# Kernel optimization log

Measured on AMD Instinct MI355X. Metric: run time of the kernel, lower is better.

## Reference

```python
import jax, jax.numpy as jnp
import numpy as np

ROWS, COLS = 10, 4
B, N = 65536, 16


def setup_inputs() -> dict:
    key = jax.random.key(0)
    kx, kc = jax.random.split(key)
    # 0.5 scale keeps trace(x^(rows+1))^cols finite in float32 (spectral radius ~2)
    x = jax.random.normal(kx, (B, N, N), dtype=jnp.float32) * 0.5
    # kaiming_normal_ on a 2D (rows, cols) tensor: std = sqrt(2 / fan_in), fan_in = cols
    coef = jax.random.normal(kc, (ROWS, COLS), dtype=jnp.float32) * np.float32(np.sqrt(2.0 / COLS))
    return {"x": x, "coef": coef}


def reference(x, coef):
    # x: [B, N, N]; coef: [rows, cols]
    rows, cols = coef.shape
    n = x.shape[-1] * x.shape[-2]  # numel per sample

    A0 = jnp.matmul(x, x)  # x^2, the first a_series entry

    def step(A, _):
        # original records trace(a_series[i]) = trace(x^(i+2)), then advances the power
        tr = jnp.trace(A, axis1=-2, axis2=-1)  # [B]
        return jnp.matmul(x, A), tr

    _, traces = jax.lax.scan(step, A0, None, length=rows)  # traces: [rows, B]
    t = traces.T  # [B, rows]

    jexp = jnp.arange(1, cols + 1, dtype=jnp.float32)  # j+1 exponents
    iexp = jnp.arange(rows, dtype=jnp.float32)
    # feature[b, i, j] = trace(x^(i+2))^(j+1) / n^(i+j+1)
    denom = jnp.float32(n) ** (iexp[:, None] + jexp[None, :])  # [rows, cols]
    feats = (t[:, :, None] ** jexp[None, None, :]) / denom  # [B, rows, cols]

    # terms = coef * feats, summed over (rows, cols) per sample -> [B]
    return jnp.einsum('rc,brc->b', coef, feats)
```

## Files before the change

### kernel.cpp

```cpp
#include <hip/hip_runtime.h>

typedef __fp16 f16x4 __attribute__((ext_vector_type(4)));
typedef __fp16 f16x2 __attribute__((ext_vector_type(2)));
typedef float f32x4 __attribute__((ext_vector_type(4)));

__device__ __forceinline__ f16x4 cat(f16x2 lo, f16x2 hi) {
    return __builtin_shufflevector(lo, hi, 0, 1, 2, 3);
}
__device__ __forceinline__ f16x2 u2h(unsigned v) {
    union { unsigned u; f16x2 h; } x; x.u = v; return x.h;
}
template <int CTRL>
__device__ __forceinline__ float dpp_add(float v) {
    int s = __builtin_amdgcn_update_dpp(0, __float_as_int(v), CTRL, 0xf, 0xf, true);
    return v + __int_as_float(s);
}

__global__ __launch_bounds__(256, 8) void acoef_kernel(
    const float* __restrict__ x,
    const float* __restrict__ coef,
    float* __restrict__ out,
    int B)
{
    const int lane = threadIdx.x & 63;
    const int wid  = (blockIdx.x * 256 + threadIdx.x) >> 6;
    const int stride = gridDim.x * 4;

    const int n = lane & 15;
    const int q = lane >> 4;
    const bool diagsel = ((n >> 2) == q);

    unsigned slo = (n == 0 ? 0x3C00u : 0u) | (n == 1 ? 0x3C000000u : 0u);
    unsigned shi = (n == 2 ? 0x3C00u : 0u) | (n == 3 ? 0x3C000000u : 0u);
    const f16x4 selB  = cat(u2h(slo), u2h(shi));
    const f16x4 onesA = cat(u2h(0x3C003C00u), u2h(0x3C003C00u));
    const f32x4 zero  = {0.f, 0.f, 0.f, 0.f};
    float4 cf[3]; float scl[3];
    #pragma unroll
    for (int p = 0; p < 3; ++p) {
        int s = 4 * p + n;
        int idx = s > 9 ? 9 : s;
        cf[p]  = *(const float4*)(coef + 4 * idx);
        scl[p] = __int_as_float((127 - 8 * s) << 23);
    }

    const int aoff = n * 16 + 4 * q;
    const int boff = 4 * q * 16 + n;

    int s = wid;
    const float* xb = x + (size_t)s * 256;
    float4 a = *(const float4*)(xb + aoff);
    float b0 = xb[boff], b1 = xb[boff + 16], b2 = xb[boff + 32], b3 = xb[boff + 48];

    while (true) {
        const int s2 = s + stride;
        const bool more = (s2 < B);
        const float* xn = x + (size_t)(more ? s2 : s) * 256;
        float4 an = *(const float4*)(xn + aoff);
        float bn0 = xn[boff], bn1 = xn[boff + 16], bn2 = xn[boff + 32], bn3 = xn[boff + 48];

        f16x4 xA = cat(__builtin_amdgcn_cvt_pkrtz(a.x, a.y),
                       __builtin_amdgcn_cvt_pkrtz(a.z, a.w));
        f16x4 xB = cat(__builtin_amdgcn_cvt_pkrtz(b0, b1),
                       __builtin_amdgcn_cvt_pkrtz(b2, b3));

        f32x4 acc = __builtin_amdgcn_mfma_f32_16x16x16f16(xA, xB, zero, 0, 0, 0);

        f16x2 prpk[6];
        float trf = 0.0f;
        #pragma unroll
        for (int st = 0; st < 10; ++st) {
            float selA = (n & 1) ? acc[1] : acc[0];
            float selBv = (n & 1) ? acc[3] : acc[2];
            float dv = (n & 2) ? selBv : selA;
            float tr = diagsel ? dv : 0.0f;
            if (st & 1) prpk[st >> 1] = __builtin_amdgcn_cvt_pkrtz(trf, tr);
            else        trf = tr;

            if (st < 9) {
                f16x4 bf = cat(__builtin_amdgcn_cvt_pkrtz(acc[0], acc[1]),
                               __builtin_amdgcn_cvt_pkrtz(acc[2], acc[3]));
                acc = __builtin_amdgcn_mfma_f32_16x16x16f16(xA, bf, zero, 0, 0, 0);
            }
        }
        prpk[5] = u2h(0u);

        float result = 0.0f;
        #pragma unroll
        for (int p = 0; p < 3; ++p) {
            f16x4 Ap = cat(prpk[2 * p], prpk[2 * p + 1]);
            f32x4 c1 = __builtin_amdgcn_mfma_f32_16x16x16f16(Ap, selB, zero, 0, 0, 0);
            f16x4 Bp = cat(__builtin_amdgcn_cvt_pkrtz(c1[0], c1[1]),
                           __builtin_amdgcn_cvt_pkrtz(c1[2], c1[3]));
            f32x4 c2 = __builtin_amdgcn_mfma_f32_16x16x16f16(onesA, Bp, zero, 0, 0, 0);
            float t = c2[0];
            float sv = t * 0x1p-8f;
            float h = fmaf(sv, cf[p].w, cf[p].z);
            h = fmaf(sv, h, cf[p].y);
            h = fmaf(sv, h, cf[p].x);
            result = fmaf(sv * h, scl[p], result);
        }
        result = dpp_add<0xB1>(result);
        result = dpp_add<0x4E>(result);
        if (lane == 0) out[s] = result;

        if (!more) break;
        s = s2; a = an; b0 = bn0; b1 = bn1; b2 = bn2; b3 = bn3;
    }
}

extern "C" void kernel_launch(void* const* d_in, const int* in_sizes, int n_in,
                              void* d_out, int out_size, void* d_ws, size_t ws_size,
                              hipStream_t stream) {
    const float* x    = (const float*)d_in[0];
    const float* coef = (const float*)d_in[1];
    float* out        = (float*)d_out;
    const int B = in_sizes[0] / 256;
    acoef_kernel<<<dim3(2048), dim3(256), 0, stream>>>(x, coef, out, B);
}
```

Baseline: 96.12 us.

## Process two samples per wave to interleave independent MFMA chains

```diff
diff --git a/kernel.cpp b/kernel.cpp
--- a/kernel.cpp
+++ b/kernel.cpp
@@ -16,7 +16,7 @@
     return v + __int_as_float(s);
 }
 
-__global__ __launch_bounds__(256, 8) void acoef_kernel(
+__global__ __launch_bounds__(256, 4) void acoef_kernel(
     const float* __restrict__ x,
     const float* __restrict__ coef,
     float* __restrict__ out,
@@ -24,7 +24,7 @@
 {
     const int lane = threadIdx.x & 63;
     const int wid  = (blockIdx.x * 256 + threadIdx.x) >> 6;
-    const int stride = gridDim.x * 4;
+    const int nw   = gridDim.x * 4;
 
     const int n = lane & 15;
     const int q = lane >> 4;
@@ -45,67 +45,95 @@
     }
 
     const int aoff = n * 16 + 4 * q;
-    const int boff = 4 * q * 16 + n;
+    const int boff = 64 * q + n;
 
-    int s = wid;
-    const float* xb = x + (size_t)s * 256;
-    float4 a = *(const float4*)(xb + aoff);
-    float b0 = xb[boff], b1 = xb[boff + 16], b2 = xb[boff + 32], b3 = xb[boff + 48];
+    const int npair = B >> 1;
+    int pp = wid;
+
+    float4 a[2], bv[2];
+    {
+        const float* x0 = x + (size_t)(2 * pp) * 256;
+        const float* x1 = x0 + 256;
+        a[0]  = *(const float4*)(x0 + aoff);
+        a[1]  = *(const float4*)(x1 + aoff);
+        bv[0] = make_float4(x0[boff], x0[boff + 16], x0[boff + 32], x0[boff + 48]);
+        bv[1] = make_float4(x1[boff], x1[boff + 16], x1[boff + 32], x1[boff + 48]);
+    }
 
     while (true) {
-        const int s2 = s + stride;
-        const bool more = (s2 < B);
-        const float* xn = x + (size_t)(more ? s2 : s) * 256;
-        float4 an = *(const float4*)(xn + aoff);
-        float bn0 = xn[boff], bn1 = xn[boff + 16], bn2 = xn[boff + 32], bn3 = xn[boff + 48];
+        const int pn = pp + nw;
+        const bool more = (pn < npair);
+        const float* y0 = x + (size_t)(2 * (more ? pn : pp)) * 256;
+        const float* y1 = y0 + 256;
+        float4 na0 = *(const float4*)(y0 + aoff);
+        float4 na1 = *(const float4*)(y1 + aoff);
+        float4 nb0 = make_float4(y0[boff], y0[boff + 16], y0[boff + 32], y0[boff + 48]);
+        float4 nb1 = make_float4(y1[boff], y1[boff + 16], y1[boff + 32], y1[boff + 48]);
 
-        f16x4 xA = cat(__builtin_amdgcn_cvt_pkrtz(a.x, a.y),
-                       __builtin_amdgcn_cvt_pkrtz(a.z, a.w));
-        f16x4 xB = cat(__builtin_amdgcn_cvt_pkrtz(b0, b1),
-                       __builtin_amdgcn_cvt_pkrtz(b2, b3));
+        f16x4 xA[2], xB[2];
+        f32x4 acc[2];
+        #pragma unroll
+        for (int c = 0; c < 2; ++c) {
+            xA[c] = cat(__builtin_amdgcn_cvt_pkrtz(a[c].x, a[c].y),
+                        __builtin_amdgcn_cvt_pkrtz(a[c].z, a[c].w));
+            xB[c] = cat(__builtin_amdgcn_cvt_pkrtz(bv[c].x, bv[c].y),
+                        __builtin_amdgcn_cvt_pkrtz(bv[c].z, bv[c].w));
+            acc[c] = __builtin_amdgcn_mfma_f32_16x16x16f16(xA[c], xB[c], zero, 0, 0, 0);
+        }
 
-        f32x4 acc = __builtin_amdgcn_mfma_f32_16x16x16f16(xA, xB, zero, 0, 0, 0);
-
-        f16x2 prpk[6];
-        float trf = 0.0f;
+        f16x2 prpk[2][6];
+        float trf[2];
         #pragma unroll
         for (int st = 0; st < 10; ++st) {
-            float selA = (n & 1) ? acc[1] : acc[0];
-            float selBv = (n & 1) ? acc[3] : acc[2];
-            float dv = (n & 2) ? selBv : selA;
-            float tr = diagsel ? dv : 0.0f;
-            if (st & 1) prpk[st >> 1] = __builtin_amdgcn_cvt_pkrtz(trf, tr);
-            else        trf = tr;
-
+            #pragma unroll
+            for (int c = 0; c < 2; ++c) {
+                float sA = (n & 1) ? acc[c][1] : acc[c][0];
+                float sB = (n & 1) ? acc[c][3] : acc[c][2];
+                float dv = (n & 2) ? sB : sA;
+                float tr = diagsel ? dv : 0.0f;
+                if (st & 1) prpk[c][st >> 1] = __builtin_amdgcn_cvt_pkrtz(trf[c], tr);
+                else        trf[c] = tr;
+            }
             if (st < 9) {
-                f16x4 bf = cat(__builtin_amdgcn_cvt_pkrtz(acc[0], acc[1]),
-                               __builtin_amdgcn_cvt_pkrtz(acc[2], acc[3]));
-                acc = __builtin_amdgcn_mfma_f32_16x16x16f16(xA, bf, zero, 0, 0, 0);
+                #pragma unroll
+                for (int c = 0; c < 2; ++c) {
+                    f16x4 bf = cat(__builtin_amdgcn_cvt_pkrtz(acc[c][0], acc[c][1]),
+                                   __builtin_amdgcn_cvt_pkrtz(acc[c][2], acc[c][3]));
+                    acc[c] = __builtin_amdgcn_mfma_f32_16x16x16f16(xA[c], bf, zero, 0, 0, 0);
+                }
             }
         }
-        prpk[5] = u2h(0u);
+        prpk[0][5] = u2h(0u);
+        prpk[1][5] = u2h(0u);
 
-        float result = 0.0f;
+        float res[2] = {0.0f, 0.0f};
         #pragma unroll
         for (int p = 0; p < 3; ++p) {
-            f16x4 Ap = cat(prpk[2 * p], prpk[2 * p + 1]);
-            f32x4 c1 = __builtin_amdgcn_mfma_f32_16x16x16f16(Ap, selB, zero, 0, 0, 0);
-            f16x4 Bp = cat(__builtin_amdgcn_cvt_pkrtz(c1[0], c1[1]),
-                           __builtin_amdgcn_cvt_pkrtz(c1[2], c1[3]));
-            f32x4 c2 = __builtin_amdgcn_mfma_f32_16x16x16f16(onesA, Bp, zero, 0, 0, 0);
-            float t = c2[0];
-            float sv = t * 0x1p-8f;
-            float h = fmaf(sv, cf[p].w, cf[p].z);
-            h = fmaf(sv, h, cf[p].y);
-            h = fmaf(sv, h, cf[p].x);
-            result = fmaf(sv * h, scl[p], result);
+            #pragma unroll
+            for (int c = 0; c < 2; ++c) {
+                f16x4 Ap = cat(prpk[c][2 * p], prpk[c][2 * p + 1]);
+                f32x4 c1 = __builtin_amdgcn_mfma_f32_16x16x16f16(Ap, selB, zero, 0, 0, 0);
+                f16x4 Bp = cat(__builtin_amdgcn_cvt_pkrtz(c1[0], c1[1]),
+                               __builtin_amdgcn_cvt_pkrtz(c1[2], c1[3]));
+                f32x4 c2 = __builtin_amdgcn_mfma_f32_16x16x16f16(onesA, Bp, zero, 0, 0, 0);
+                float t = c2[0];
+                float sv = t * 0x1p-8f;
+                float h = fmaf(sv, cf[p].w, cf[p].z);
+                h = fmaf(sv, h, cf[p].y);
+                h = fmaf(sv, h, cf[p].x);
+                res[c] = fmaf(sv * h, scl[p], res[c]);
+            }
         }
-        result = dpp_add<0xB1>(result);
-        result = dpp_add<0x4E>(result);
-        if (lane == 0) out[s] = result;
+        #pragma unroll
+        for (int c = 0; c < 2; ++c) {
+            res[c] = dpp_add<0xB1>(res[c]);
+            res[c] = dpp_add<0x4E>(res[c]);
+        }
+        if (lane == 0) *(float2*)(out + 2 * pp) = make_float2(res[0], res[1]);
 
         if (!more) break;
-        s = s2; a = an; b0 = bn0; b1 = bn1; b2 = bn2; b3 = bn3;
+        pp = pn;
+        a[0] = na0; a[1] = na1; bv[0] = nb0; bv[1] = nb1;
     }
 }
 
@@ -116,5 +144,5 @@
     const float* coef = (const float*)d_in[1];
     float* out        = (float*)d_out;
     const int B = in_sizes[0] / 256;
-    acoef_kernel<<<dim3(2048), dim3(256), 0, stream>>>(x, coef, out, B);
+    acoef_kernel<<<dim3(1024), dim3(256), 0, stream>>>(x, coef, out, B);
 }
```

Measured after the change: 100.2 us. +4.2%, slower.

## Launch one wave per sample and transpose x via identity MFMA

Applied to the files above, without the earlier changes.

```diff
diff --git a/kernel.cpp b/kernel.cpp
--- a/kernel.cpp
+++ b/kernel.cpp
@@ -16,25 +16,32 @@
     return v + __int_as_float(s);
 }
 
-__global__ __launch_bounds__(256, 8) void acoef_kernel(
+__global__ __launch_bounds__(256, 6) void acoef_kernel(
     const float* __restrict__ x,
     const float* __restrict__ coef,
-    float* __restrict__ out,
-    int B)
+    float* __restrict__ out)
 {
     const int lane = threadIdx.x & 63;
-    const int wid  = (blockIdx.x * 256 + threadIdx.x) >> 6;
-    const int stride = gridDim.x * 4;
+    const int b = (blockIdx.x * 256 + (int)threadIdx.x) >> 6;
 
     const int n = lane & 15;
     const int q = lane >> 4;
     const bool diagsel = ((n >> 2) == q);
 
+    const float4 a = *(const float4*)(x + (size_t)b * 256 + n * 16 + 4 * q);
+
+    unsigned ilo = 0, ihi = 0;
+    if (diagsel) {
+        ilo = ((n & 3) == 0 ? 0x3C00u : 0u) | ((n & 3) == 1 ? 0x3C000000u : 0u);
+        ihi = ((n & 3) == 2 ? 0x3C00u : 0u) | ((n & 3) == 3 ? 0x3C000000u : 0u);
+    }
+    const f16x4 idB = cat(u2h(ilo), u2h(ihi));
     unsigned slo = (n == 0 ? 0x3C00u : 0u) | (n == 1 ? 0x3C000000u : 0u);
     unsigned shi = (n == 2 ? 0x3C00u : 0u) | (n == 3 ? 0x3C000000u : 0u);
     const f16x4 selB  = cat(u2h(slo), u2h(shi));
     const f16x4 onesA = cat(u2h(0x3C003C00u), u2h(0x3C003C00u));
     const f32x4 zero  = {0.f, 0.f, 0.f, 0.f};
+
     float4 cf[3]; float scl[3];
     #pragma unroll
     for (int p = 0; p < 3; ++p) {
@@ -44,69 +51,51 @@
         scl[p] = __int_as_float((127 - 8 * s) << 23);
     }
 
-    const int aoff = n * 16 + 4 * q;
-    const int boff = 4 * q * 16 + n;
+    f16x4 xA = cat(__builtin_amdgcn_cvt_pkrtz(a.x, a.y),
+                   __builtin_amdgcn_cvt_pkrtz(a.z, a.w));
+    f32x4 d = __builtin_amdgcn_mfma_f32_16x16x16f16(xA, idB, zero, 0, 0, 0);
+    f16x4 xB = cat(__builtin_amdgcn_cvt_pkrtz(d[0], d[1]),
+                   __builtin_amdgcn_cvt_pkrtz(d[2], d[3]));
 
-    int s = wid;
-    const float* xb = x + (size_t)s * 256;
-    float4 a = *(const float4*)(xb + aoff);
-    float b0 = xb[boff], b1 = xb[boff + 16], b2 = xb[boff + 32], b3 = xb[boff + 48];
+    f32x4 acc = __builtin_amdgcn_mfma_f32_16x16x16f16(xA, xB, zero, 0, 0, 0);
 
-    while (true) {
-        const int s2 = s + stride;
-        const bool more = (s2 < B);
-        const float* xn = x + (size_t)(more ? s2 : s) * 256;
-        float4 an = *(const float4*)(xn + aoff);
-        float bn0 = xn[boff], bn1 = xn[boff + 16], bn2 = xn[boff + 32], bn3 = xn[boff + 48];
+    f16x2 prpk[6];
+    float trf = 0.0f;
+    #pragma unroll
+    for (int st = 0; st < 10; ++st) {
+        float sA = (n & 1) ? acc[1] : acc[0];
+        float sB = (n & 1) ? acc[3] : acc[2];
+        float dv = (n & 2) ? sB : sA;
+        float tr = diagsel ? dv : 0.0f;
+        if (st & 1) prpk[st >> 1] = __builtin_amdgcn_cvt_pkrtz(trf, tr);
+        else        trf = tr;
 
-        f16x4 xA = cat(__builtin_amdgcn_cvt_pkrtz(a.x, a.y),
-                       __builtin_amdgcn_cvt_pkrtz(a.z, a.w));
-        f16x4 xB = cat(__builtin_amdgcn_cvt_pkrtz(b0, b1),
-                       __builtin_amdgcn_cvt_pkrtz(b2, b3));
+        if (st < 9) {
+            f16x4 bf = cat(__builtin_amdgcn_cvt_pkrtz(acc[0], acc[1]),
+                           __builtin_amdgcn_cvt_pkrtz(acc[2], acc[3]));
+            acc = __builtin_amdgcn_mfma_f32_16x16x16f16(xA, bf, zero, 0, 0, 0);
+        }
+    }
+    prpk[5] = u2h(0u);
 
-        f32x4 acc = __builtin_amdgcn_mfma_f32_16x16x16f16(xA, xB, zero, 0, 0, 0);
-
-        f16x2 prpk[6];
-        float trf = 0.0f;
-        #pragma unroll
-        for (int st = 0; st < 10; ++st) {
-            float selA = (n & 1) ? acc[1] : acc[0];
-            float selBv = (n & 1) ? acc[3] : acc[2];
-            float dv = (n & 2) ? selBv : selA;
-            float tr = diagsel ? dv : 0.0f;
-            if (st & 1) prpk[st >> 1] = __builtin_amdgcn_cvt_pkrtz(trf, tr);
-            else        trf = tr;
-
-            if (st < 9) {
-                f16x4 bf = cat(__builtin_amdgcn_cvt_pkrtz(acc[0], acc[1]),
-                               __builtin_amdgcn_cvt_pkrtz(acc[2], acc[3]));
-                acc = __builtin_amdgcn_mfma_f32_16x16x16f16(xA, bf, zero, 0, 0, 0);
-            }
-        }
-        prpk[5] = u2h(0u);
-
-        float result = 0.0f;
-        #pragma unroll
-        for (int p = 0; p < 3; ++p) {
-            f16x4 Ap = cat(prpk[2 * p], prpk[2 * p + 1]);
-            f32x4 c1 = __builtin_amdgcn_mfma_f32_16x16x16f16(Ap, selB, zero, 0, 0, 0);
-            f16x4 Bp = cat(__builtin_amdgcn_cvt_pkrtz(c1[0], c1[1]),
-                           __builtin_amdgcn_cvt_pkrtz(c1[2], c1[3]));
-            f32x4 c2 = __builtin_amdgcn_mfma_f32_16x16x16f16(onesA, Bp, zero, 0, 0, 0);
-            float t = c2[0];
-            float sv = t * 0x1p-8f;
-            float h = fmaf(sv, cf[p].w, cf[p].z);
-            h = fmaf(sv, h, cf[p].y);
-            h = fmaf(sv, h, cf[p].x);
-            result = fmaf(sv * h, scl[p], result);
-        }
-        result = dpp_add<0xB1>(result);
-        result = dpp_add<0x4E>(result);
-        if (lane == 0) out[s] = result;
-
-        if (!more) break;
-        s = s2; a = an; b0 = bn0; b1 = bn1; b2 = bn2; b3 = bn3;
+    float result = 0.0f;
+    #pragma unroll
+    for (int p = 0; p < 3; ++p) {
+        f16x4 Ap = cat(prpk[2 * p], prpk[2 * p + 1]);
+        f32x4 c1 = __builtin_amdgcn_mfma_f32_16x16x16f16(Ap, selB, zero, 0, 0, 0);
+        f16x4 Bp = cat(__builtin_amdgcn_cvt_pkrtz(c1[0], c1[1]),
+                       __builtin_amdgcn_cvt_pkrtz(c1[2], c1[3]));
+        f32x4 c2 = __builtin_amdgcn_mfma_f32_16x16x16f16(onesA, Bp, zero, 0, 0, 0);
+        float t = c2[0];
+        float sv = t * 0x1p-8f;
+        float h = fmaf(sv, cf[p].w, cf[p].z);
+        h = fmaf(sv, h, cf[p].y);
+        h = fmaf(sv, h, cf[p].x);
+        result = fmaf(sv * h, scl[p], result);
     }
+    result = dpp_add<0xB1>(result);
+    result = dpp_add<0x4E>(result);
+    if (lane == 0) out[b] = result;
 }
 
 extern "C" void kernel_launch(void* const* d_in, const int* in_sizes, int n_in,
@@ -116,5 +105,5 @@
     const float* coef = (const float*)d_in[1];
     float* out        = (float*)d_out;
     const int B = in_sizes[0] / 256;
-    acoef_kernel<<<dim3(2048), dim3(256), 0, stream>>>(x, coef, out, B);
+    acoef_kernel<<<dim3(B / 4), dim3(256), 0, stream>>>(x, coef, out);
 }
```

Result: no change. 97.13 us (+1.1%).
